# Kernel optimization log

Measured on AMD Instinct MI355X. Metric: run time of the kernel, lower is better.

Reference implementation:

```python
import jax, jax.numpy as jnp
import numpy as np

POOL = 14        # pool_size (init kwarg)
STRIDE = 16.0    # hard-coded feature stride in the original call()


def setup_inputs() -> dict:
    key = jax.random.key(0)
    k1, k2, k3 = jax.random.split(key, 3)
    H = W = 128
    C = 1024
    N = 256
    image = jax.random.normal(k1, (1, H, W, C), dtype=jnp.float32)
    img_px = H * 16  # original image resolution implied by stride 16
    # boxes: (x_center, y_center, w, h) in image pixels, guaranteed in-bounds after /16 rounding
    wh = jax.random.uniform(k2, (N, 2), minval=160.0, maxval=480.0)
    xy = jax.random.uniform(k3, (N, 2)) * (img_px - wh - 64.0) + wh / 2.0 + 32.0
    rois = jnp.concatenate([xy, wh], axis=1).astype(jnp.float32)
    return {"image": image, "RoI_inImage": rois}


def _axis_coords(start, size, out_size, limit):
    """TF2 tf.image.resize bilinear (half-pixel centers) sample coords for a
    crop [start, start+size) resized to out_size, vectorized over RoIs.
    Returns (i0, i1, t): lower/upper gather indices into the full feature map
    and the lerp weight. Matches TF: lerp uses unclamped floor, indices clamped."""
    scale = size[:, None].astype(jnp.float32) / out_size          # [N,1]
    src = (jnp.arange(out_size, dtype=jnp.float32) + 0.5)[None, :] * scale - 0.5  # [N,P]
    fl = jnp.floor(src)
    t = src - fl
    hi = (size[:, None] - 1).astype(jnp.float32)
    i0 = jnp.clip(fl, 0.0, hi).astype(jnp.int32) + start[:, None]
    i1 = jnp.clip(fl + 1.0, 0.0, hi).astype(jnp.int32) + start[:, None]
    i0 = jnp.clip(i0, 0, limit - 1)
    i1 = jnp.clip(i1, 0, limit - 1)
    return i0, i1, t


def _roi_pool(image, rois):
    H, W = image.shape[1], image.shape[2]
    feat = image[0]  # [H,W,C]
    x, y, w, h = rois[:, 0], rois[:, 1], rois[:, 2], rois[:, 3]
    # integer crop in feature-map coords, exactly as the original rounding
    r = jnp.round((x - w / 2.0) / STRIDE).astype(jnp.int32)   # col start
    c = jnp.round((y - h / 2.0) / STRIDE).astype(jnp.int32)   # row start
    wf = jnp.maximum(jnp.round(w / STRIDE).astype(jnp.int32), 1)
    hf = jnp.maximum(jnp.round(h / STRIDE).astype(jnp.int32), 1)
    y0, y1, ty = _axis_coords(c, hf, POOL, H)  # rows
    x0, x1, tx = _axis_coords(r, wf, POOL, W)  # cols
    # four bilinear corner gathers: [N,P,P,C]
    v00 = feat[y0[:, :, None], x0[:, None, :]]
    v01 = feat[y0[:, :, None], x1[:, None, :]]
    v10 = feat[y1[:, :, None], x0[:, None, :]]
    v11 = feat[y1[:, :, None], x1[:, None, :]]
    ty = ty[:, :, None, None]
    tx = tx[:, None, :, None]
    out = (v00 * (1.0 - ty) + v10 * ty) * (1.0 - tx) + (v01 * (1.0 - ty) + v11 * ty) * tx
    return out[None]  # [1, N, P, P, C]


def reference(image, RoI_inImage):
    return _roi_pool(image, RoI_inImage)
```

## Files before the change

### kernel.cpp

```cpp
#include <hip/hip_runtime.h>


#define H_ 128
#define W_ 128
#define C_ 1024
#define POOL_ 14
#define NROI_ 256
#define NPIX_ (NROI_ * POOL_ * POOL_)
#define NR_ (NROI_ * POOL_)
#define NBINS_ 128
#define CHUNKJ_ (NPIX_ / 8)

typedef float f32x4 __attribute__((ext_vector_type(4)));

__device__ __forceinline__ int row_y0(const float* __restrict__ rois, int rid) {
    const int n  = rid / POOL_;
    const int yj = rid % POOL_;
    const float y = rois[n * 4 + 1];
    const float h = rois[n * 4 + 3];
    const int c  = (int)rintf((y - h * 0.5f) / 16.0f);
    const int hf = max((int)rintf(h / 16.0f), 1);
    const float scy  = (float)hf / (float)POOL_;
    const float srcy = ((float)yj + 0.5f) * scy - 0.5f;
    const float fly  = floorf(srcy);
    int y0 = (int)fminf(fmaxf(fly, 0.0f), (float)(hf - 1)) + c;
    return min(max(y0, 0), H_ - 1);
}

__global__ __launch_bounds__(256) void sort_rows(
    const float* __restrict__ rois, int* __restrict__ ws)
{
    __shared__ int hist[NBINS_];
    __shared__ int off[NBINS_];
    const int tid = threadIdx.x;
    if (tid < NBINS_) hist[tid] = 0;
    __syncthreads();
    #pragma unroll
    for (int rid = tid; rid < NR_; rid += 256)
        atomicAdd(&hist[row_y0(rois, rid)], 1);
    __syncthreads();
    if (tid == 0) {
        int run = 0;
        for (int i = 0; i < NBINS_; ++i) { off[i] = run; run += hist[i]; }
    }
    __syncthreads();
    #pragma unroll
    for (int rid = tid; rid < NR_; rid += 256) {
        const int b = row_y0(rois, rid);
        const int pos = atomicAdd(&off[b], 1);
        ws[pos] = rid;
    }
}

__global__ __launch_bounds__(256) void roi_pool_sorted(
    const float* __restrict__ feat, const float* __restrict__ rois,
    float* __restrict__ out, const int* __restrict__ ws)
{
    const int q   = (blockIdx.x & 7) * CHUNKJ_ + (blockIdx.x >> 3);
    const int rq  = q / POOL_;
    const int xj  = q - rq * POOL_;
    const int rid = ws[rq];
    const int yj  = rid % POOL_;
    const int n   = rid / POOL_;

    const float x = rois[n * 4 + 0];
    const float y = rois[n * 4 + 1];
    const float w = rois[n * 4 + 2];
    const float h = rois[n * 4 + 3];

    const int r_  = (int)rintf((x - w * 0.5f) / 16.0f);
    const int c_  = (int)rintf((y - h * 0.5f) / 16.0f);
    const int wf = max((int)rintf(w / 16.0f), 1);
    const int hf = max((int)rintf(h / 16.0f), 1);

    const float scy  = (float)hf / (float)POOL_;
    const float srcy = ((float)yj + 0.5f) * scy - 0.5f;
    const float fly  = floorf(srcy);
    const float ty   = srcy - fly;
    const float hiy  = (float)(hf - 1);
    int y0 = (int)fminf(fmaxf(fly, 0.0f), hiy) + c_;
    int y1 = (int)fminf(fmaxf(fly + 1.0f, 0.0f), hiy) + c_;
    y0 = min(max(y0, 0), H_ - 1);
    y1 = min(max(y1, 0), H_ - 1);

    const float scx  = (float)wf / (float)POOL_;
    const float srcx = ((float)xj + 0.5f) * scx - 0.5f;
    const float flx  = floorf(srcx);
    const float tx   = srcx - flx;
    const float hix  = (float)(wf - 1);
    int x0 = (int)fminf(fmaxf(flx, 0.0f), hix) + r_;
    int x1 = (int)fminf(fmaxf(flx + 1.0f, 0.0f), hix) + r_;
    x0 = min(max(x0, 0), W_ - 1);
    x1 = min(max(x1, 0), W_ - 1);

    const f32x4* __restrict__ p00 = (const f32x4*)(feat + ((size_t)y0 * W_ + x0) * C_);
    const f32x4* __restrict__ p01 = (const f32x4*)(feat + ((size_t)y0 * W_ + x1) * C_);
    const f32x4* __restrict__ p10 = (const f32x4*)(feat + ((size_t)y1 * W_ + x0) * C_);
    const f32x4* __restrict__ p11 = (const f32x4*)(feat + ((size_t)y1 * W_ + x1) * C_);
    f32x4* __restrict__ po =
        (f32x4*)(out + (((size_t)n * (POOL_ * POOL_)) + (size_t)yj * POOL_ + xj) * C_);

    const int tid = threadIdx.x;

    const f32x4 v00 = p00[tid];
    const f32x4 v01 = p01[tid];
    const f32x4 v10 = p10[tid];
    const f32x4 v11 = p11[tid];

    const float omty = 1.0f - ty;
    const float omtx = 1.0f - tx;

    f32x4 o = (v00 * omty + v10 * ty) * omtx + (v01 * omty + v11 * ty) * tx;

    __builtin_nontemporal_store(o, &po[tid]);
}

__global__ __launch_bounds__(256) void roi_pool_direct(
    const float* __restrict__ feat, const float* __restrict__ rois,
    float* __restrict__ out)
{
    const int bid = blockIdx.x;
    const int blk = (bid % 8) * (NPIX_ / 8) + bid / 8;

    const int xj = blk % POOL_;
    const int yj = (blk / POOL_) % POOL_;
    const int n  = blk / (POOL_ * POOL_);

    const float x = rois[n * 4 + 0];
    const float y = rois[n * 4 + 1];
    const float w = rois[n * 4 + 2];
    const float h = rois[n * 4 + 3];

    const int r_  = (int)rintf((x - w * 0.5f) / 16.0f);
    const int c_  = (int)rintf((y - h * 0.5f) / 16.0f);
    const int wf = max((int)rintf(w / 16.0f), 1);
    const int hf = max((int)rintf(h / 16.0f), 1);

    const float scy  = (float)hf / (float)POOL_;
    const float srcy = ((float)yj + 0.5f) * scy - 0.5f;
    const float fly  = floorf(srcy);
    const float ty   = srcy - fly;
    const float hiy  = (float)(hf - 1);
    int y0 = (int)fminf(fmaxf(fly, 0.0f), hiy) + c_;
    int y1 = (int)fminf(fmaxf(fly + 1.0f, 0.0f), hiy) + c_;
    y0 = min(max(y0, 0), H_ - 1);
    y1 = min(max(y1, 0), H_ - 1);

    const float scx  = (float)wf / (float)POOL_;
    const float srcx = ((float)xj + 0.5f) * scx - 0.5f;
    const float flx  = floorf(srcx);
    const float tx   = srcx - flx;
    const float hix  = (float)(wf - 1);
    int x0 = (int)fminf(fmaxf(flx, 0.0f), hix) + r_;
    int x1 = (int)fminf(fmaxf(flx + 1.0f, 0.0f), hix) + r_;
    x0 = min(max(x0, 0), W_ - 1);
    x1 = min(max(x1, 0), W_ - 1);

    const f32x4* __restrict__ p00 = (const f32x4*)(feat + ((size_t)y0 * W_ + x0) * C_);
    const f32x4* __restrict__ p01 = (const f32x4*)(feat + ((size_t)y0 * W_ + x1) * C_);
    const f32x4* __restrict__ p10 = (const f32x4*)(feat + ((size_t)y1 * W_ + x0) * C_);
    const f32x4* __restrict__ p11 = (const f32x4*)(feat + ((size_t)y1 * W_ + x1) * C_);
    f32x4* __restrict__ po = (f32x4*)(out + (size_t)blk * C_);

    const int tid = threadIdx.x;
    const f32x4 v00 = p00[tid];
    const f32x4 v01 = p01[tid];
    const f32x4 v10 = p10[tid];
    const f32x4 v11 = p11[tid];

    const float omty = 1.0f - ty;
    const float omtx = 1.0f - tx;
    f32x4 o = (v00 * omty + v10 * ty) * omtx + (v01 * omty + v11 * ty) * tx;
    __builtin_nontemporal_store(o, &po[tid]);
}

extern "C" void kernel_launch(void* const* d_in, const int* in_sizes, int n_in,
                              void* d_out, int out_size, void* d_ws, size_t ws_size,
                              hipStream_t stream) {
    const float* feat = (const float*)d_in[0];
    const float* rois = (const float*)d_in[1];
    float* out = (float*)d_out;

    if (ws_size < (size_t)NR_ * sizeof(int)) {
        roi_pool_direct<<<NPIX_, 256, 0, stream>>>(feat, rois, out);
        return;
    }

    int* ws = (int*)d_ws;
    sort_rows<<<1, 256, 0, stream>>>(rois, ws);
    roi_pool_sorted<<<NPIX_, 256, 0, stream>>>(feat, rois, out, ws);
}
```

Measured before the change: 61.60 us.

## Process a full output row per block with precomputed per-row records

The sort kernel now writes an 8-int record per output row holding the row indices, the y weight and the x-axis parameters, so the pooling kernel no longer recomputes ROI geometry. Each block now produces all 14 output pixels of one pooled row instead of a single pixel, cutting the block count 14x and letting neighbouring gathers within a block reuse cached feature rows. This adds serial work per block and fewer blocks for latency hiding. It also needs a larger workspace, and when that is unavailable it falls back to the direct kernel.

```diff
diff --git a/kernel.cpp b/kernel.cpp
--- a/kernel.cpp
+++ b/kernel.cpp
@@ -9,23 +9,11 @@
 #define NPIX_ (NROI_ * POOL_ * POOL_)
 #define NR_ (NROI_ * POOL_)
 #define NBINS_ 128
-#define CHUNKJ_ (NPIX_ / 8)
+#define CHUNKR_ (NR_ / 8)
+#define RECW_ 8
+#define WS_INTS (NR_ * RECW_)
 
 typedef float f32x4 __attribute__((ext_vector_type(4)));
-
-__device__ __forceinline__ int row_y0(const float* __restrict__ rois, int rid) {
-    const int n  = rid / POOL_;
-    const int yj = rid % POOL_;
-    const float y = rois[n * 4 + 1];
-    const float h = rois[n * 4 + 3];
-    const int c  = (int)rintf((y - h * 0.5f) / 16.0f);
-    const int hf = max((int)rintf(h / 16.0f), 1);
-    const float scy  = (float)hf / (float)POOL_;
-    const float srcy = ((float)yj + 0.5f) * scy - 0.5f;
-    const float fly  = floorf(srcy);
-    int y0 = (int)fminf(fmaxf(fly, 0.0f), (float)(hf - 1)) + c;
-    return min(max(y0, 0), H_ - 1);
-}
 
 __global__ __launch_bounds__(256) void sort_rows(
     const float* __restrict__ rois, int* __restrict__ ws)
@@ -35,33 +23,121 @@
     const int tid = threadIdx.x;
     if (tid < NBINS_) hist[tid] = 0;
     __syncthreads();
-    #pragma unroll
-    for (int rid = tid; rid < NR_; rid += 256)
-        atomicAdd(&hist[row_y0(rois, rid)], 1);
+
+    for (int rid = tid; rid < NR_; rid += 256) {
+        const int n  = rid / POOL_;
+        const int yj = rid % POOL_;
+        const float y = rois[n * 4 + 1];
+        const float h = rois[n * 4 + 3];
+        const int c  = (int)rintf((y - h * 0.5f) / 16.0f);
+        const int hf = max((int)rintf(h / 16.0f), 1);
+        const float scy  = (float)hf / (float)POOL_;
+        const float srcy = ((float)yj + 0.5f) * scy - 0.5f;
+        const float fly  = floorf(srcy);
+        int y0 = (int)fminf(fmaxf(fly, 0.0f), (float)(hf - 1)) + c;
+        y0 = min(max(y0, 0), H_ - 1);
+        atomicAdd(&hist[y0], 1);
+    }
     __syncthreads();
     if (tid == 0) {
         int run = 0;
         for (int i = 0; i < NBINS_; ++i) { off[i] = run; run += hist[i]; }
     }
     __syncthreads();
-    #pragma unroll
+
     for (int rid = tid; rid < NR_; rid += 256) {
-        const int b = row_y0(rois, rid);
-        const int pos = atomicAdd(&off[b], 1);
-        ws[pos] = rid;
-    }
-}
-
-__global__ __launch_bounds__(256) void roi_pool_sorted(
+        const int n  = rid / POOL_;
+        const int yj = rid % POOL_;
+        const float x = rois[n * 4 + 0];
+        const float y = rois[n * 4 + 1];
+        const float w = rois[n * 4 + 2];
+        const float h = rois[n * 4 + 3];
+
+        const int r_  = (int)rintf((x - w * 0.5f) / 16.0f);
+        const int c_  = (int)rintf((y - h * 0.5f) / 16.0f);
+        const int wf = max((int)rintf(w / 16.0f), 1);
+        const int hf = max((int)rintf(h / 16.0f), 1);
+
+        const float scy  = (float)hf / (float)POOL_;
+        const float srcy = ((float)yj + 0.5f) * scy - 0.5f;
+        const float fly  = floorf(srcy);
+        const float ty   = srcy - fly;
+        const float hiy  = (float)(hf - 1);
+        int y0 = (int)fminf(fmaxf(fly, 0.0f), hiy) + c_;
+        int y1 = (int)fminf(fmaxf(fly + 1.0f, 0.0f), hiy) + c_;
+        y0 = min(max(y0, 0), H_ - 1);
+        y1 = min(max(y1, 0), H_ - 1);
+
+        const int pos = atomicAdd(&off[y0], 1);
+        int* rec = ws + pos * RECW_;
+        rec[0] = rid;
+        rec[1] = y0;
+        rec[2] = y1;
+        ((float*)rec)[3] = ty;
+        rec[4] = r_;
+        ((float*)rec)[5] = (float)wf / (float)POOL_;
+        ((float*)rec)[6] = (float)(wf - 1);
+        rec[7] = 0;
+    }
+}
+
+__global__ __launch_bounds__(256) void roi_pool_rows(
+    const float* __restrict__ feat, float* __restrict__ out,
+    const int* __restrict__ ws)
+{
+    const int pos = (blockIdx.x & 7) * CHUNKR_ + (blockIdx.x >> 3);
+    const int* rec = ws + pos * RECW_;
+    const int   rid = rec[0];
+    const int   y0  = rec[1];
+    const int   y1  = rec[2];
+    const float ty  = ((const float*)rec)[3];
+    const int   r_  = rec[4];
+    const float scx = ((const float*)rec)[5];
+    const float hix = ((const float*)rec)[6];
+
+    const int n  = rid / POOL_;
+    const int yj = rid % POOL_;
+
+    const float* __restrict__ row0 = feat + (size_t)y0 * (W_ * C_);
+    const float* __restrict__ row1 = feat + (size_t)y1 * (W_ * C_);
+    float* __restrict__ orow =
+        out + ((size_t)n * (POOL_ * POOL_) + (size_t)yj * POOL_) * C_;
+
+    const int tid = threadIdx.x;
+    const float omty = 1.0f - ty;
+
+    #pragma unroll 2
+    for (int xj = 0; xj < POOL_; ++xj) {
+        const float srcx = ((float)xj + 0.5f) * scx - 0.5f;
+        const float flx  = floorf(srcx);
+        const float tx   = srcx - flx;
+        int x0 = (int)fminf(fmaxf(flx, 0.0f), hix) + r_;
+        int x1 = (int)fminf(fmaxf(flx + 1.0f, 0.0f), hix) + r_;
+        x0 = min(max(x0, 0), W_ - 1);
+        x1 = min(max(x1, 0), W_ - 1);
+
+        const f32x4 v00 = ((const f32x4*)(row0 + (size_t)x0 * C_))[tid];
+        const f32x4 v01 = ((const f32x4*)(row0 + (size_t)x1 * C_))[tid];
+        const f32x4 v10 = ((const f32x4*)(row1 + (size_t)x0 * C_))[tid];
+        const f32x4 v11 = ((const f32x4*)(row1 + (size_t)x1 * C_))[tid];
+
+        const float omtx = 1.0f - tx;
+        f32x4 o = (v00 * omty + v10 * ty) * omtx + (v01 * omty + v11 * ty) * tx;
+
+        __builtin_nontemporal_store(o, (f32x4*)(orow + (size_t)xj * C_) + tid);
+    }
+}
+
+__global__ __launch_bounds__(256) void roi_pool_direct(
     const float* __restrict__ feat, const float* __restrict__ rois,
-    float* __restrict__ out, const int* __restrict__ ws)
+    float* __restrict__ out)
 {
-    const int q   = (blockIdx.x & 7) * CHUNKJ_ + (blockIdx.x >> 3);
-    const int rq  = q / POOL_;
-    const int xj  = q - rq * POOL_;
-    const int rid = ws[rq];
-    const int yj  = rid % POOL_;
-    const int n   = rid / POOL_;
+    const int bid = blockIdx.x;
+    const int blk = (bid % 8) * (NPIX_ / 8) + bid / 8;
+
+    const int xj = blk % POOL_;
+    const int yj = (blk / POOL_) % POOL_;
+    const int n  = blk / (POOL_ * POOL_);
 
     const float x = rois[n * 4 + 0];
     const float y = rois[n * 4 + 1];
@@ -97,69 +173,6 @@
     const f32x4* __restrict__ p01 = (const f32x4*)(feat + ((size_t)y0 * W_ + x1) * C_);
     const f32x4* __restrict__ p10 = (const f32x4*)(feat + ((size_t)y1 * W_ + x0) * C_);
     const f32x4* __restrict__ p11 = (const f32x4*)(feat + ((size_t)y1 * W_ + x1) * C_);
-    f32x4* __restrict__ po =
-        (f32x4*)(out + (((size_t)n * (POOL_ * POOL_)) + (size_t)yj * POOL_ + xj) * C_);
-
-    const int tid = threadIdx.x;
-
-    const f32x4 v00 = p00[tid];
-    const f32x4 v01 = p01[tid];
-    const f32x4 v10 = p10[tid];
-    const f32x4 v11 = p11[tid];
-
-    const float omty = 1.0f - ty;
-    const float omtx = 1.0f - tx;
-
-    f32x4 o = (v00 * omty + v10 * ty) * omtx + (v01 * omty + v11 * ty) * tx;
-
-    __builtin_nontemporal_store(o, &po[tid]);
-}
-
-__global__ __launch_bounds__(256) void roi_pool_direct(
-    const float* __restrict__ feat, const float* __restrict__ rois,
-    float* __restrict__ out)
-{
-    const int bid = blockIdx.x;
-    const int blk = (bid % 8) * (NPIX_ / 8) + bid / 8;
-
-    const int xj = blk % POOL_;
-    const int yj = (blk / POOL_) % POOL_;
-    const int n  = blk / (POOL_ * POOL_);
-
-    const float x = rois[n * 4 + 0];
-    const float y = rois[n * 4 + 1];
-    const float w = rois[n * 4 + 2];
-    const float h = rois[n * 4 + 3];
-
-    const int r_  = (int)rintf((x - w * 0.5f) / 16.0f);
-    const int c_  = (int)rintf((y - h * 0.5f) / 16.0f);
-    const int wf = max((int)rintf(w / 16.0f), 1);
-    const int hf = max((int)rintf(h / 16.0f), 1);
-
-    const float scy  = (float)hf / (float)POOL_;
-    const float srcy = ((float)yj + 0.5f) * scy - 0.5f;
-    const float fly  = floorf(srcy);
-    const float ty   = srcy - fly;
-    const float hiy  = (float)(hf - 1);
-    int y0 = (int)fminf(fmaxf(fly, 0.0f), hiy) + c_;
-    int y1 = (int)fminf(fmaxf(fly + 1.0f, 0.0f), hiy) + c_;
-    y0 = min(max(y0, 0), H_ - 1);
-    y1 = min(max(y1, 0), H_ - 1);
-
-    const float scx  = (float)wf / (float)POOL_;
-    const float srcx = ((float)xj + 0.5f) * scx - 0.5f;
-    const float flx  = floorf(srcx);
-    const float tx   = srcx - flx;
-    const float hix  = (float)(wf - 1);
-    int x0 = (int)fminf(fmaxf(flx, 0.0f), hix) + r_;
-    int x1 = (int)fminf(fmaxf(flx + 1.0f, 0.0f), hix) + r_;
-    x0 = min(max(x0, 0), W_ - 1);
-    x1 = min(max(x1, 0), W_ - 1);
-
-    const f32x4* __restrict__ p00 = (const f32x4*)(feat + ((size_t)y0 * W_ + x0) * C_);
-    const f32x4* __restrict__ p01 = (const f32x4*)(feat + ((size_t)y0 * W_ + x1) * C_);
-    const f32x4* __restrict__ p10 = (const f32x4*)(feat + ((size_t)y1 * W_ + x0) * C_);
-    const f32x4* __restrict__ p11 = (const f32x4*)(feat + ((size_t)y1 * W_ + x1) * C_);
     f32x4* __restrict__ po = (f32x4*)(out + (size_t)blk * C_);
 
     const int tid = threadIdx.x;
@@ -181,12 +194,12 @@
     const float* rois = (const float*)d_in[1];
     float* out = (float*)d_out;
 
-    if (ws_size < (size_t)NR_ * sizeof(int)) {
+    if (ws_size < (size_t)WS_INTS * sizeof(int)) {
         roi_pool_direct<<<NPIX_, 256, 0, stream>>>(feat, rois, out);
         return;
     }
 
     int* ws = (int*)d_ws;
     sort_rows<<<1, 256, 0, stream>>>(rois, ws);
-    roi_pool_sorted<<<NPIX_, 256, 0, stream>>>(feat, rois, out, ws);
-}
+    roi_pool_rows<<<NR_, 256, 0, stream>>>(feat, out, ws);
+}
```

New measurement: 60.11 us. 2.4% less time.
